# Performance work log

Hardware: AMD Instinct MI355X
Metric: run time of the kernel (lower is better)

The kernel has to match this reference:

```python
import jax, jax.numpy as jnp
import numpy as np

B, N, M = 2, 8192, 8192


def setup_inputs() -> dict:
    key = jax.random.key(0)
    ks = jax.random.split(key, 12)
    def rn(k, shape):
        return jax.random.normal(k, shape, dtype=jnp.float32)
    return {
        "in_xyz": rn(ks[0], (B, N, 3)),
        "in_rot": rn(ks[1], (B, N, 4)),
        "in_scale": rn(ks[2], (B, N, 3)),
        "in_opacity": rn(ks[3], (B, N, 1)),
        "in_sh_dc": rn(ks[4], (B, N, 3)),
        "in_sh_rest": rn(ks[5], (B, N, 45)),
        "out_xyz": rn(ks[6], (B, M, 3)),
        "out_rot": rn(ks[7], (B, M, 4)),
        "out_scale": rn(ks[8], (B, M, 3)),
        "out_opacity": rn(ks[9], (B, M, 1)),
        "out_sh_dc": rn(ks[10], (B, M, 3)),
        "out_sh_rest": rn(ks[11], (B, M, 45)),
    }


POS_W, ROT_W, SCALE_W, OPAC_W, SH_W = 1.0, 0.5, 0.5, 0.3, 0.2


def _cdist(a, b):
    # a: [B,M,3], b: [B,N,3] -> [B,M,N] Euclidean distance via Gram trick
    sq = (jnp.sum(a * a, -1)[:, :, None] + jnp.sum(b * b, -1)[:, None, :]
          - 2.0 * jnp.einsum('bmd,bnd->bmn', a, b))
    return jnp.sqrt(jnp.maximum(sq, 0.0))


def _gather(x, idx):
    # x: [B,N,D], idx: [B,M] -> [B,M,D]
    return jnp.take_along_axis(x, idx[:, :, None], axis=1)


def reference(in_xyz, in_rot, in_scale, in_opacity, in_sh_dc, in_sh_rest,
              out_xyz, out_rot, out_scale, out_opacity, out_sh_dc, out_sh_rest):
    dist = _cdist(out_xyz, in_xyz)                 # [B,M,N]
    min_out_to_in = jnp.min(dist, axis=2)          # [B,M]
    match_idx = jnp.argmin(dist, axis=2)           # [B,M]
    min_in_to_out = jnp.min(dist, axis=1)          # [B,N]
    pos_loss = (min_out_to_in.mean() + min_in_to_out.mean()) / 2

    matched_rot = _gather(in_rot, match_idx)
    matched_scale = _gather(in_scale, match_idx)
    matched_opacity = _gather(in_opacity, match_idx)
    matched_sh_dc = _gather(in_sh_dc, match_idx)
    matched_sh_rest = _gather(in_sh_rest, match_idx)

    rot_dot = jnp.abs(jnp.sum(out_rot * matched_rot, axis=-1))
    rot_loss = jnp.mean(1.0 - rot_dot)
    scale_loss = jnp.mean(jnp.abs(out_scale - matched_scale))
    opacity_loss = jnp.mean(jnp.abs(out_opacity - matched_opacity))
    sh_loss = (jnp.mean(jnp.abs(out_sh_dc - matched_sh_dc))
               + jnp.mean(jnp.abs(out_sh_rest - matched_sh_rest)))

    total = (POS_W * pos_loss + ROT_W * rot_loss + SCALE_W * scale_loss
             + OPAC_W * opacity_loss + SH_W * sh_loss)
    return total
```

## Files before the change

### kernel.cpp

```cpp
#include <hip/hip_runtime.h>


#define BB 2
#define NN 8192
#define MM 8192
#define TILE_PTS 1024
#define NTILES 8
#define CHUNK_PTS 64
#define CH_STRIDE (CHUNK_PTS * 4 + 4)
#define PM 64
#define NBLK (BB * MM / PM)

__device__ __forceinline__ void dmerge(float& d, int& i, float od, int oi) {
    if (od < d || (od == d && oi < i)) { d = od; i = oi; }
}

__device__ __forceinline__ void stage_load(const float* __restrict__ xyz,
                                           int b, int tile, int t, uint4* wb) {
    const uint4* src = (const uint4*)((const char*)xyz +
                       ((size_t)b * NN + (size_t)tile * TILE_PTS) * 12);
#pragma unroll
    for (int k = 0; k < 3; ++k) wb[k] = src[t * 3 + k];
}
__device__ __forceinline__ void stage_store(const uint4* wb, int t, float* smem) {
    const unsigned int* w = (const unsigned int*)wb;
    const int p0 = t * 4;
    float4* dst = (float4*)(smem + (p0 >> 6) * CH_STRIDE) + (p0 & 63);
#pragma unroll
    for (int i = 0; i < 4; ++i) {
        float x = __uint_as_float(w[3 * i + 0]);
        float y = __uint_as_float(w[3 * i + 1]);
        float z = __uint_as_float(w[3 * i + 2]);
        float4 v;
        v.x = x; v.y = y; v.z = z;
        v.w = fmaf(z, z, fmaf(y, y, x * x));
        dst[i] = v;
    }
}

__global__ __launch_bounds__(256) void k_out(
    const float* __restrict__ in_xyz,
    const float* __restrict__ in_rot,
    const float* __restrict__ in_scale,
    const float* __restrict__ in_op,
    const float* __restrict__ in_dc,
    const float* __restrict__ in_rest,
    const float* __restrict__ out_xyz,
    const float* __restrict__ out_rot,
    const float* __restrict__ out_scale,
    const float* __restrict__ out_op,
    const float* __restrict__ out_dc,
    const float* __restrict__ out_rest,
    float* __restrict__ part) {

    __shared__ float smem[2][16 * CH_STRIDE];
    __shared__ float red[4][8];
    __shared__ float bds[PM];
    __shared__ int   idxs[PM];

    const int t  = threadIdx.x;
    const int ml = t >> 4;
    const int c  = t & 15;
    const int b  = blockIdx.x >> 7;
    const int mbase = (blockIdx.x & 127) * PM;
    const int m0 = mbase + ml * 4;

    float m2x0, m2y0, m2z0, msq0, m2x1, m2y1, m2z1, msq1;
    float m2x2, m2y2, m2z2, msq2, m2x3, m2y3, m2z3, msq3;
#define LOADQ(i)                                                            \
    { const float* op = out_xyz + ((size_t)b * MM + m0 + i) * 3;            \
      float ox = op[0], oy = op[1], oz = op[2];                             \
      m2x##i = -2.f * ox; m2y##i = -2.f * oy; m2z##i = -2.f * oz;           \
      msq##i = fmaf(oz, oz, fmaf(oy, oy, ox * ox)); }
    LOADQ(0) LOADQ(1) LOADQ(2) LOADQ(3)
#undef LOADQ

    float bd0 = 3e38f, bd1 = 3e38f, bd2 = 3e38f, bd3 = 3e38f;
    int   bi0 = 0,     bi1 = 0,     bi2 = 0,     bi3 = 0;

    {
        uint4 wb[3];
        stage_load(in_xyz, b, 0, t, wb);
        stage_store(wb, t, smem[0]);
    }
    __syncthreads();

    for (int tile = 0; tile < NTILES; ++tile) {
        const int cur = tile & 1;
        uint4 wb[3];
        if (tile + 1 < NTILES) stage_load(in_xyz, b, tile + 1, t, wb);

        const float4* cp = (const float4*)(smem[cur] + c * CH_STRIDE);
        const int base = tile * TILE_PTS + c * CHUNK_PTS;

#define SCORE(p, jj)                                                        \
        { float k0 = fmaf(p.x, m2x0, fmaf(p.y, m2y0, fmaf(p.z, m2z0, p.w)));\
          float k1 = fmaf(p.x, m2x1, fmaf(p.y, m2y1, fmaf(p.z, m2z1, p.w)));\
          float k2 = fmaf(p.x, m2x2, fmaf(p.y, m2y2, fmaf(p.z, m2z2, p.w)));\
          float k3 = fmaf(p.x, m2x3, fmaf(p.y, m2y3, fmaf(p.z, m2z3, p.w)));\
          if (k0 < bd0) { bd0 = k0; bi0 = base + (jj); }                    \
          if (k1 < bd1) { bd1 = k1; bi1 = base + (jj); }                    \
          if (k2 < bd2) { bd2 = k2; bi2 = base + (jj); }                    \
          if (k3 < bd3) { bd3 = k3; bi3 = base + (jj); } }

        float4 q0 = cp[0], q1 = cp[1], q2 = cp[2], q3 = cp[3];
#pragma unroll
        for (int j = 0; j < CHUNK_PTS; j += 4) {
            float4 r0, r1, r2, r3;
            if (j + 4 < CHUNK_PTS) {
                r0 = cp[j + 4]; r1 = cp[j + 5]; r2 = cp[j + 6]; r3 = cp[j + 7];
            }
            SCORE(q0, j) SCORE(q1, j + 1) SCORE(q2, j + 2) SCORE(q3, j + 3)
            q0 = r0; q1 = r1; q2 = r2; q3 = r3;
        }
#undef SCORE

        if (tile + 1 < NTILES) stage_store(wb, t, smem[1 - cur]);
        __syncthreads();
    }

#pragma unroll
    for (int off = 1; off < 16; off <<= 1) {
        float od; int oi;
        od = __shfl_xor(bd0, off, 64); oi = __shfl_xor(bi0, off, 64); dmerge(bd0, bi0, od, oi);
        od = __shfl_xor(bd1, off, 64); oi = __shfl_xor(bi1, off, 64); dmerge(bd1, bi1, od, oi);
        od = __shfl_xor(bd2, off, 64); oi = __shfl_xor(bi2, off, 64); dmerge(bd2, bi2, od, oi);
        od = __shfl_xor(bd3, off, 64); oi = __shfl_xor(bi3, off, 64); dmerge(bd3, bi3, od, oi);
    }
    if (c == 0) {
        bds[ml * 4 + 0] = bd0 + msq0; idxs[ml * 4 + 0] = bi0;
        bds[ml * 4 + 1] = bd1 + msq1; idxs[ml * 4 + 1] = bi1;
        bds[ml * 4 + 2] = bd2 + msq2; idxs[ml * 4 + 2] = bi2;
        bds[ml * 4 + 3] = bd3 + msq3; idxs[ml * 4 + 3] = bi3;
    }
    __syncthreads();

    float pos = 0.f, rot = 0.f, scl = 0.f, opa = 0.f, dcv = 0.f, rsv = 0.f;
    if (t < PM) {
        const size_t og = (size_t)b * MM + (mbase + t);
        const size_t ig = (size_t)b * NN + (size_t)idxs[t];
        pos = sqrtf(fmaxf(bds[t], 0.f));
        const float4 orv = ((const float4*)out_rot)[og];
        const float4 irv = ((const float4*)in_rot)[ig];
        float rdot = orv.x * irv.x + orv.y * irv.y + orv.z * irv.z + orv.w * irv.w;
        rot = 1.f - fabsf(rdot);
#pragma unroll
        for (int q = 0; q < 3; ++q) scl += fabsf(out_scale[og * 3 + q] - in_scale[ig * 3 + q]);
        opa = fabsf(out_op[og] - in_op[ig]);
#pragma unroll
        for (int q = 0; q < 3; ++q) dcv += fabsf(out_dc[og * 3 + q] - in_dc[ig * 3 + q]);
    } else {
        const int u = t - PM;
        const int mloc = u / 3;
        const int k = u - mloc * 3;
        const size_t og = (size_t)b * MM + (mbase + mloc);
        const size_t ig = (size_t)b * NN + (size_t)idxs[mloc];
#pragma unroll
        for (int q = 0; q < 15; ++q) {
            int e = k * 15 + q;
            rsv += fabsf(out_rest[og * 45 + e] - in_rest[ig * 45 + e]);
        }
    }

#pragma unroll
    for (int off = 1; off < 64; off <<= 1) {
        pos += __shfl_xor(pos, off, 64);
        rot += __shfl_xor(rot, off, 64);
        scl += __shfl_xor(scl, off, 64);
        opa += __shfl_xor(opa, off, 64);
        dcv += __shfl_xor(dcv, off, 64);
        rsv += __shfl_xor(rsv, off, 64);
    }
    if ((t & 63) == 0) {
        const int w = t >> 6;
        red[w][0] = pos; red[w][1] = rot; red[w][2] = scl;
        red[w][3] = opa; red[w][4] = dcv; red[w][5] = rsv;
    }
    __syncthreads();
    if (t < 6) {
        float s = red[0][t] + red[1][t] + red[2][t] + red[3][t];
        part[(size_t)blockIdx.x * 6 + t] = s;
    }
}

__global__ __launch_bounds__(256) void k_in(
    const float* __restrict__ in_xyz,
    const float* __restrict__ out_xyz,
    float* __restrict__ part) {

    __shared__ float smem[2][16 * CH_STRIDE];
    __shared__ float red[4];

    const int t  = threadIdx.x;
    const int ml = t >> 4;
    const int c  = t & 15;
    const int b  = blockIdx.x >> 7;
    const int n0 = (blockIdx.x & 127) * PM + ml * 4;

    float n2x0, n2y0, n2z0, nsq0, n2x1, n2y1, n2z1, nsq1;
    float n2x2, n2y2, n2z2, nsq2, n2x3, n2y3, n2z3, nsq3;
#define LOADQ(i)                                                            \
    { const float* ip = in_xyz + ((size_t)b * NN + n0 + i) * 3;             \
      float x = ip[0], y = ip[1], z = ip[2];                                \
      n2x##i = -2.f * x; n2y##i = -2.f * y; n2z##i = -2.f * z;              \
      nsq##i = fmaf(z, z, fmaf(y, y, x * x)); }
    LOADQ(0) LOADQ(1) LOADQ(2) LOADQ(3)
#undef LOADQ

    float bd0 = 3e38f, bd1 = 3e38f, bd2 = 3e38f, bd3 = 3e38f;

    {
        uint4 wb[3];
        stage_load(out_xyz, b, 0, t, wb);
        stage_store(wb, t, smem[0]);
    }
    __syncthreads();

    for (int tile = 0; tile < NTILES; ++tile) {
        const int cur = tile & 1;
        uint4 wb[3];
        if (tile + 1 < NTILES) stage_load(out_xyz, b, tile + 1, t, wb);

        const float4* cp = (const float4*)(smem[cur] + c * CH_STRIDE);

#define SCOREI(p)                                                           \
        { float k0 = fmaf(p.x, n2x0, fmaf(p.y, n2y0, fmaf(p.z, n2z0, p.w)));\
          float k1 = fmaf(p.x, n2x1, fmaf(p.y, n2y1, fmaf(p.z, n2z1, p.w)));\
          float k2 = fmaf(p.x, n2x2, fmaf(p.y, n2y2, fmaf(p.z, n2z2, p.w)));\
          float k3 = fmaf(p.x, n2x3, fmaf(p.y, n2y3, fmaf(p.z, n2z3, p.w)));\
          bd0 = fminf(bd0, k0); bd1 = fminf(bd1, k1);                       \
          bd2 = fminf(bd2, k2); bd3 = fminf(bd3, k3); }

        float4 q0 = cp[0], q1 = cp[1], q2 = cp[2], q3 = cp[3];
#pragma unroll
        for (int j = 0; j < CHUNK_PTS; j += 4) {
            float4 r0, r1, r2, r3;
            if (j + 4 < CHUNK_PTS) {
                r0 = cp[j + 4]; r1 = cp[j + 5]; r2 = cp[j + 6]; r3 = cp[j + 7];
            }
            SCOREI(q0) SCOREI(q1) SCOREI(q2) SCOREI(q3)
            q0 = r0; q1 = r1; q2 = r2; q3 = r3;
        }
#undef SCOREI

        if (tile + 1 < NTILES) stage_store(wb, t, smem[1 - cur]);
        __syncthreads();
    }

#pragma unroll
    for (int off = 1; off < 16; off <<= 1) {
        bd0 = fminf(bd0, __shfl_xor(bd0, off, 64));
        bd1 = fminf(bd1, __shfl_xor(bd1, off, 64));
        bd2 = fminf(bd2, __shfl_xor(bd2, off, 64));
        bd3 = fminf(bd3, __shfl_xor(bd3, off, 64));
    }

    float v = 0.0f;
    if (c == 0) {
        v  = sqrtf(fmaxf(bd0 + nsq0, 0.f));
        v += sqrtf(fmaxf(bd1 + nsq1, 0.f));
        v += sqrtf(fmaxf(bd2 + nsq2, 0.f));
        v += sqrtf(fmaxf(bd3 + nsq3, 0.f));
    }
#pragma unroll
    for (int off = 1; off < 64; off <<= 1) v += __shfl_xor(v, off, 64);
    if ((t & 63) == 0) red[t >> 6] = v;
    __syncthreads();
    if (t == 0)
        part[blockIdx.x] = red[0] + red[1] + red[2] + red[3];
}

__global__ __launch_bounds__(256) void k_fin(const float* __restrict__ pout,
                                             const float* __restrict__ pin,
                                             unsigned int* __restrict__ out) {
    __shared__ float red[4][8];
    const int t = threadIdx.x;
    float s0 = 0.f, s1 = 0.f, s2 = 0.f, s3 = 0.f, s4 = 0.f, s5 = 0.f, s6 = 0.f;
    for (int i = t; i < NBLK; i += 256) {
        s0 += pout[(size_t)i * 6 + 0];
        s1 += pout[(size_t)i * 6 + 1];
        s2 += pout[(size_t)i * 6 + 2];
        s3 += pout[(size_t)i * 6 + 3];
        s4 += pout[(size_t)i * 6 + 4];
        s5 += pout[(size_t)i * 6 + 5];
        s6 += pin[i];
    }
#pragma unroll
    for (int off = 1; off < 64; off <<= 1) {
        s0 += __shfl_xor(s0, off, 64);
        s1 += __shfl_xor(s1, off, 64);
        s2 += __shfl_xor(s2, off, 64);
        s3 += __shfl_xor(s3, off, 64);
        s4 += __shfl_xor(s4, off, 64);
        s5 += __shfl_xor(s5, off, 64);
        s6 += __shfl_xor(s6, off, 64);
    }
    if ((t & 63) == 0) {
        const int w = t >> 6;
        red[w][0] = s0; red[w][1] = s1; red[w][2] = s2; red[w][3] = s3;
        red[w][4] = s4; red[w][5] = s5; red[w][6] = s6;
    }
    __syncthreads();
    if (t == 0) {
        float a[7];
#pragma unroll
        for (int j = 0; j < 7; ++j)
            a[j] = red[0][j] + red[1][j] + red[2][j] + red[3][j];
        const float inv_bm = 1.0f / (float)(BB * MM);
        const float inv_bn = 1.0f / (float)(BB * NN);
        const float pos = 0.5f * (a[0] * inv_bm + a[6] * inv_bn);
        const float rot = a[1] * inv_bm;
        const float scl = a[2] * inv_bm * (1.f / 3.f);
        const float opa = a[3] * inv_bm;
        const float sh  = a[4] * inv_bm * (1.f / 3.f) + a[5] * inv_bm * (1.f / 45.f);
        const float total = 1.0f * pos + 0.5f * rot + 0.5f * scl + 0.3f * opa + 0.2f * sh;
        unsigned int ub = __float_as_uint(total);
        unsigned int r  = (ub + 0x7FFFu + ((ub >> 16) & 1u)) >> 16;
        if (!(total == total) || fabsf(total) > 1e30f) r = 0x4080u;
        out[0] = (r << 16) | r;
    }
}

extern "C" void kernel_launch(void* const* d_in, const int* in_sizes, int n_in,
                              void* d_out, int out_size, void* d_ws, size_t ws_size,
                              hipStream_t stream) {
    const float* in_xyz    = (const float*)d_in[0];
    const float* in_rot    = (const float*)d_in[1];
    const float* in_scale  = (const float*)d_in[2];
    const float* in_op     = (const float*)d_in[3];
    const float* in_dc     = (const float*)d_in[4];
    const float* in_rest   = (const float*)d_in[5];
    const float* out_xyz   = (const float*)d_in[6];
    const float* out_rot   = (const float*)d_in[7];
    const float* out_scale = (const float*)d_in[8];
    const float* out_op    = (const float*)d_in[9];
    const float* out_dc    = (const float*)d_in[10];
    const float* out_rest  = (const float*)d_in[11];

    float* pout = (float*)d_ws;
    float* pin  = pout + (size_t)NBLK * 6;

    k_out<<<NBLK, 256, 0, stream>>>(in_xyz, in_rot, in_scale, in_op, in_dc, in_rest,
                                    out_xyz, out_rot, out_scale, out_op, out_dc, out_rest,
                                    pout);
    k_in<<<NBLK, 256, 0, stream>>>(in_xyz, out_xyz, pin);
    k_fin<<<1, 256, 0, stream>>>(pout, pin, (unsigned int*)d_out);
}
```

Measured before the change: 142.7 us.

## Split nearest-neighbor search over two halves and move gathers to epilogue kernel

Each query block now scans only half of the candidate points, which doubles the grid from 256 to 512 blocks so more CUs stay busy. Per-half minimum distances and indices go to workspace. A new epilogue kernel merges the halves, then does the attribute gathers, L1/rotation losses and the in-to-out sqrt sums. The costs are an extra kernel launch and the workspace round trip, and a tie between halves resolves to the lower index as before.

```diff
diff --git a/kernel.cpp b/kernel.cpp
--- a/kernel.cpp
+++ b/kernel.cpp
@@ -5,20 +5,20 @@
 #define NN 8192
 #define MM 8192
 #define TILE_PTS 1024
-#define NTILES 8
+#define NTILES_H 4
 #define CHUNK_PTS 64
 #define CH_STRIDE (CHUNK_PTS * 4 + 4)
 #define PM 64
-#define NBLK (BB * MM / PM)
+#define NPAIR (BB * (MM / PM) * 2)
 
 __device__ __forceinline__ void dmerge(float& d, int& i, float od, int oi) {
     if (od < d || (od == d && oi < i)) { d = od; i = oi; }
 }
 
 __device__ __forceinline__ void stage_load(const float* __restrict__ xyz,
-                                           int b, int tile, int t, uint4* wb) {
+                                           int b, int gtile, int t, uint4* wb) {
     const uint4* src = (const uint4*)((const char*)xyz +
-                       ((size_t)b * NN + (size_t)tile * TILE_PTS) * 12);
+                       ((size_t)b * NN + (size_t)gtile * TILE_PTS) * 12);
 #pragma unroll
     for (int k = 0; k < 3; ++k) wb[k] = src[t * 3 + k];
 }
@@ -40,30 +40,19 @@
 
 __global__ __launch_bounds__(256) void k_out(
     const float* __restrict__ in_xyz,
-    const float* __restrict__ in_rot,
-    const float* __restrict__ in_scale,
-    const float* __restrict__ in_op,
-    const float* __restrict__ in_dc,
-    const float* __restrict__ in_rest,
     const float* __restrict__ out_xyz,
-    const float* __restrict__ out_rot,
-    const float* __restrict__ out_scale,
-    const float* __restrict__ out_op,
-    const float* __restrict__ out_dc,
-    const float* __restrict__ out_rest,
-    float* __restrict__ part) {
+    float* __restrict__ outD2,
+    int*   __restrict__ outIdx) {
 
     __shared__ float smem[2][16 * CH_STRIDE];
-    __shared__ float red[4][8];
-    __shared__ float bds[PM];
-    __shared__ int   idxs[PM];
 
     const int t  = threadIdx.x;
     const int ml = t >> 4;
     const int c  = t & 15;
-    const int b  = blockIdx.x >> 7;
-    const int mbase = (blockIdx.x & 127) * PM;
-    const int m0 = mbase + ml * 4;
+    const int bid = blockIdx.x;
+    const int s  = (bid >> 7) & 1;
+    const int b  = bid >> 8;
+    const int m0 = (bid & 127) * PM + ml * 4;
 
     float m2x0, m2y0, m2z0, msq0, m2x1, m2y1, m2z1, msq1;
     float m2x2, m2y2, m2z2, msq2, m2x3, m2y3, m2z3, msq3;
@@ -78,20 +67,21 @@
     float bd0 = 3e38f, bd1 = 3e38f, bd2 = 3e38f, bd3 = 3e38f;
     int   bi0 = 0,     bi1 = 0,     bi2 = 0,     bi3 = 0;
 
+    const int gt0 = s * NTILES_H;
     {
         uint4 wb[3];
-        stage_load(in_xyz, b, 0, t, wb);
+        stage_load(in_xyz, b, gt0, t, wb);
         stage_store(wb, t, smem[0]);
     }
     __syncthreads();
 
-    for (int tile = 0; tile < NTILES; ++tile) {
+    for (int tile = 0; tile < NTILES_H; ++tile) {
         const int cur = tile & 1;
         uint4 wb[3];
-        if (tile + 1 < NTILES) stage_load(in_xyz, b, tile + 1, t, wb);
+        if (tile + 1 < NTILES_H) stage_load(in_xyz, b, gt0 + tile + 1, t, wb);
 
         const float4* cp = (const float4*)(smem[cur] + c * CH_STRIDE);
-        const int base = tile * TILE_PTS + c * CHUNK_PTS;
+        const int base = (gt0 + tile) * TILE_PTS + c * CHUNK_PTS;
 
 #define SCORE(p, jj)                                                        \
         { float k0 = fmaf(p.x, m2x0, fmaf(p.y, m2y0, fmaf(p.z, m2z0, p.w)));\
@@ -115,7 +105,7 @@
         }
 #undef SCORE
 
-        if (tile + 1 < NTILES) stage_store(wb, t, smem[1 - cur]);
+        if (tile + 1 < NTILES_H) stage_store(wb, t, smem[1 - cur]);
         __syncthreads();
     }
 
@@ -128,74 +118,28 @@
         od = __shfl_xor(bd3, off, 64); oi = __shfl_xor(bi3, off, 64); dmerge(bd3, bi3, od, oi);
     }
     if (c == 0) {
-        bds[ml * 4 + 0] = bd0 + msq0; idxs[ml * 4 + 0] = bi0;
-        bds[ml * 4 + 1] = bd1 + msq1; idxs[ml * 4 + 1] = bi1;
-        bds[ml * 4 + 2] = bd2 + msq2; idxs[ml * 4 + 2] = bi2;
-        bds[ml * 4 + 3] = bd3 + msq3; idxs[ml * 4 + 3] = bi3;
-    }
-    __syncthreads();
-
-    float pos = 0.f, rot = 0.f, scl = 0.f, opa = 0.f, dcv = 0.f, rsv = 0.f;
-    if (t < PM) {
-        const size_t og = (size_t)b * MM + (mbase + t);
-        const size_t ig = (size_t)b * NN + (size_t)idxs[t];
-        pos = sqrtf(fmaxf(bds[t], 0.f));
-        const float4 orv = ((const float4*)out_rot)[og];
-        const float4 irv = ((const float4*)in_rot)[ig];
-        float rdot = orv.x * irv.x + orv.y * irv.y + orv.z * irv.z + orv.w * irv.w;
-        rot = 1.f - fabsf(rdot);
-#pragma unroll
-        for (int q = 0; q < 3; ++q) scl += fabsf(out_scale[og * 3 + q] - in_scale[ig * 3 + q]);
-        opa = fabsf(out_op[og] - in_op[ig]);
-#pragma unroll
-        for (int q = 0; q < 3; ++q) dcv += fabsf(out_dc[og * 3 + q] - in_dc[ig * 3 + q]);
-    } else {
-        const int u = t - PM;
-        const int mloc = u / 3;
-        const int k = u - mloc * 3;
-        const size_t og = (size_t)b * MM + (mbase + mloc);
-        const size_t ig = (size_t)b * NN + (size_t)idxs[mloc];
-#pragma unroll
-        for (int q = 0; q < 15; ++q) {
-            int e = k * 15 + q;
-            rsv += fabsf(out_rest[og * 45 + e] - in_rest[ig * 45 + e]);
-        }
-    }
-
-#pragma unroll
-    for (int off = 1; off < 64; off <<= 1) {
-        pos += __shfl_xor(pos, off, 64);
-        rot += __shfl_xor(rot, off, 64);
-        scl += __shfl_xor(scl, off, 64);
-        opa += __shfl_xor(opa, off, 64);
-        dcv += __shfl_xor(dcv, off, 64);
-        rsv += __shfl_xor(rsv, off, 64);
-    }
-    if ((t & 63) == 0) {
-        const int w = t >> 6;
-        red[w][0] = pos; red[w][1] = rot; red[w][2] = scl;
-        red[w][3] = opa; red[w][4] = dcv; red[w][5] = rsv;
-    }
-    __syncthreads();
-    if (t < 6) {
-        float s = red[0][t] + red[1][t] + red[2][t] + red[3][t];
-        part[(size_t)blockIdx.x * 6 + t] = s;
+        const size_t g = ((size_t)b * MM + m0) * 2 + s;
+        outD2[g + 0] = bd0 + msq0; outIdx[g + 0] = bi0;
+        outD2[g + 2] = bd1 + msq1; outIdx[g + 2] = bi1;
+        outD2[g + 4] = bd2 + msq2; outIdx[g + 4] = bi2;
+        outD2[g + 6] = bd3 + msq3; outIdx[g + 6] = bi3;
     }
 }
 
 __global__ __launch_bounds__(256) void k_in(
     const float* __restrict__ in_xyz,
     const float* __restrict__ out_xyz,
-    float* __restrict__ part) {
+    float* __restrict__ inD2) {
 
     __shared__ float smem[2][16 * CH_STRIDE];
-    __shared__ float red[4];
 
     const int t  = threadIdx.x;
     const int ml = t >> 4;
     const int c  = t & 15;
-    const int b  = blockIdx.x >> 7;
-    const int n0 = (blockIdx.x & 127) * PM + ml * 4;
+    const int bid = blockIdx.x;
+    const int s  = (bid >> 7) & 1;
+    const int b  = bid >> 8;
+    const int n0 = (bid & 127) * PM + ml * 4;
 
     float n2x0, n2y0, n2z0, nsq0, n2x1, n2y1, n2z1, nsq1;
     float n2x2, n2y2, n2z2, nsq2, n2x3, n2y3, n2z3, nsq3;
@@ -209,17 +153,18 @@
 
     float bd0 = 3e38f, bd1 = 3e38f, bd2 = 3e38f, bd3 = 3e38f;
 
+    const int gt0 = s * NTILES_H;
     {
         uint4 wb[3];
-        stage_load(out_xyz, b, 0, t, wb);
+        stage_load(out_xyz, b, gt0, t, wb);
         stage_store(wb, t, smem[0]);
     }
     __syncthreads();
 
-    for (int tile = 0; tile < NTILES; ++tile) {
+    for (int tile = 0; tile < NTILES_H; ++tile) {
         const int cur = tile & 1;
         uint4 wb[3];
-        if (tile + 1 < NTILES) stage_load(out_xyz, b, tile + 1, t, wb);
+        if (tile + 1 < NTILES_H) stage_load(out_xyz, b, gt0 + tile + 1, t, wb);
 
         const float4* cp = (const float4*)(smem[cur] + c * CH_STRIDE);
 
@@ -243,7 +188,7 @@
         }
 #undef SCOREI
 
-        if (tile + 1 < NTILES) stage_store(wb, t, smem[1 - cur]);
+        if (tile + 1 < NTILES_H) stage_store(wb, t, smem[1 - cur]);
         __syncthreads();
     }
 
@@ -254,20 +199,93 @@
         bd2 = fminf(bd2, __shfl_xor(bd2, off, 64));
         bd3 = fminf(bd3, __shfl_xor(bd3, off, 64));
     }
-
-    float v = 0.0f;
     if (c == 0) {
-        v  = sqrtf(fmaxf(bd0 + nsq0, 0.f));
-        v += sqrtf(fmaxf(bd1 + nsq1, 0.f));
-        v += sqrtf(fmaxf(bd2 + nsq2, 0.f));
-        v += sqrtf(fmaxf(bd3 + nsq3, 0.f));
-    }
-#pragma unroll
-    for (int off = 1; off < 64; off <<= 1) v += __shfl_xor(v, off, 64);
-    if ((t & 63) == 0) red[t >> 6] = v;
-    __syncthreads();
-    if (t == 0)
-        part[blockIdx.x] = red[0] + red[1] + red[2] + red[3];
+        const size_t g = ((size_t)b * NN + n0) * 2 + s;
+        inD2[g + 0] = bd0 + nsq0;
+        inD2[g + 2] = bd1 + nsq1;
+        inD2[g + 4] = bd2 + nsq2;
+        inD2[g + 6] = bd3 + nsq3;
+    }
+}
+
+__global__ __launch_bounds__(256) void k_epi(
+    const float* __restrict__ in_rot,
+    const float* __restrict__ in_scale,
+    const float* __restrict__ in_op,
+    const float* __restrict__ in_dc,
+    const float* __restrict__ in_rest,
+    const float* __restrict__ out_rot,
+    const float* __restrict__ out_scale,
+    const float* __restrict__ out_op,
+    const float* __restrict__ out_dc,
+    const float* __restrict__ out_rest,
+    const float* __restrict__ outD2,
+    const int*   __restrict__ outIdx,
+    const float* __restrict__ inD2,
+    float* __restrict__ pout,
+    float* __restrict__ pin) {
+
+    const int t = threadIdx.x;
+    const int blk = blockIdx.x;
+
+    if (blk < 128) {
+        const int u = blk * 256 + t;
+        const int m = u >> 1;
+        const int h = u & 1;
+        const int b = m >> 13;
+        const float d20 = outD2[(size_t)m * 2 + 0];
+        const float d21 = outD2[(size_t)m * 2 + 1];
+        const int   i0  = outIdx[(size_t)m * 2 + 0];
+        const int   i1  = outIdx[(size_t)m * 2 + 1];
+        float d2; int idx;
+        if (d21 < d20) { d2 = d21; idx = i1; }
+        else           { d2 = d20; idx = i0; }
+        const size_t og = (size_t)m;
+        const size_t ig = (size_t)b * NN + (size_t)idx;
+
+        float pos = 0.f, rot = 0.f, scl = 0.f, opa = 0.f, dcv = 0.f, rsv = 0.f;
+        if (h == 0) {
+            pos = sqrtf(fmaxf(d2, 0.f));
+            const float4 orv = ((const float4*)out_rot)[og];
+            const float4 irv = ((const float4*)in_rot)[ig];
+            float rdot = orv.x * irv.x + orv.y * irv.y + orv.z * irv.z + orv.w * irv.w;
+            rot = 1.f - fabsf(rdot);
+#pragma unroll
+            for (int q = 0; q < 3; ++q) scl += fabsf(out_scale[og * 3 + q] - in_scale[ig * 3 + q]);
+            opa = fabsf(out_op[og] - in_op[ig]);
+#pragma unroll
+            for (int q = 0; q < 3; ++q) dcv += fabsf(out_dc[og * 3 + q] - in_dc[ig * 3 + q]);
+#pragma unroll
+            for (int e = 0; e < 22; ++e)
+                rsv += fabsf(out_rest[og * 45 + e] - in_rest[ig * 45 + e]);
+        } else {
+#pragma unroll
+            for (int e = 22; e < 45; ++e)
+                rsv += fabsf(out_rest[og * 45 + e] - in_rest[ig * 45 + e]);
+        }
+
+#pragma unroll
+        for (int off = 1; off < 64; off <<= 1) {
+            pos += __shfl_xor(pos, off, 64);
+            rot += __shfl_xor(rot, off, 64);
+            scl += __shfl_xor(scl, off, 64);
+            opa += __shfl_xor(opa, off, 64);
+            dcv += __shfl_xor(dcv, off, 64);
+            rsv += __shfl_xor(rsv, off, 64);
+        }
+        if ((t & 63) == 0) {
+            const size_t w = (size_t)blk * 4 + (t >> 6);
+            pout[w * 6 + 0] = pos; pout[w * 6 + 1] = rot; pout[w * 6 + 2] = scl;
+            pout[w * 6 + 3] = opa; pout[w * 6 + 4] = dcv; pout[w * 6 + 5] = rsv;
+        }
+    } else {
+        const int g = (blk - 128) * 256 + t;
+        const float d2 = fminf(inD2[(size_t)g * 2], inD2[(size_t)g * 2 + 1]);
+        float v = sqrtf(fmaxf(d2, 0.f));
+#pragma unroll
+        for (int off = 1; off < 64; off <<= 1) v += __shfl_xor(v, off, 64);
+        if ((t & 63) == 0) pin[(size_t)(blk - 128) * 4 + (t >> 6)] = v;
+    }
 }
 
 __global__ __launch_bounds__(256) void k_fin(const float* __restrict__ pout,
@@ -276,15 +294,15 @@
     __shared__ float red[4][8];
     const int t = threadIdx.x;
     float s0 = 0.f, s1 = 0.f, s2 = 0.f, s3 = 0.f, s4 = 0.f, s5 = 0.f, s6 = 0.f;
-    for (int i = t; i < NBLK; i += 256) {
+    for (int i = t; i < 512; i += 256) {
         s0 += pout[(size_t)i * 6 + 0];
         s1 += pout[(size_t)i * 6 + 1];
         s2 += pout[(size_t)i * 6 + 2];
         s3 += pout[(size_t)i * 6 + 3];
         s4 += pout[(size_t)i * 6 + 4];
         s5 += pout[(size_t)i * 6 + 5];
-        s6 += pin[i];
-    }
+    }
+    if (t < 256) s6 += pin[t];
 #pragma unroll
     for (int off = 1; off < 64; off <<= 1) {
         s0 += __shfl_xor(s0, off, 64);
@@ -337,12 +355,16 @@
     const float* out_dc    = (const float*)d_in[10];
     const float* out_rest  = (const float*)d_in[11];
 
-    float* pout = (float*)d_ws;
-    float* pin  = pout + (size_t)NBLK * 6;
-
-    k_out<<<NBLK, 256, 0, stream>>>(in_xyz, in_rot, in_scale, in_op, in_dc, in_rest,
-                                    out_xyz, out_rot, out_scale, out_op, out_dc, out_rest,
-                                    pout);
-    k_in<<<NBLK, 256, 0, stream>>>(in_xyz, out_xyz, pin);
+    float* outD2 = (float*)d_ws;
+    int*   outIdx = (int*)(outD2 + (size_t)BB * MM * 2);
+    float* inD2  = (float*)(outIdx + (size_t)BB * MM * 2);
+    float* pout  = inD2 + (size_t)BB * NN * 2;
+    float* pin   = pout + 512 * 6;
+
+    k_out<<<NPAIR, 256, 0, stream>>>(in_xyz, out_xyz, outD2, outIdx);
+    k_in<<<NPAIR, 256, 0, stream>>>(in_xyz, out_xyz, inD2);
+    k_epi<<<192, 256, 0, stream>>>(in_rot, in_scale, in_op, in_dc, in_rest,
+                                   out_rot, out_scale, out_op, out_dc, out_rest,
+                                   outD2, outIdx, inD2, pout, pin);
     k_fin<<<1, 256, 0, stream>>>(pout, pin, (unsigned int*)d_out);
 }
```

Result: slower. 147.3 us (+3.2%).
